# Performance work log

Hardware: AMD Instinct MI355X
Metric: run time of the kernel (lower is better)

The kernel has to match this reference:

```python
import jax, jax.numpy as jnp
import numpy as np

R, C, CH, BA = 2048, 1024, 8, 8
EPS = 1e-10


def setup_inputs() -> dict:
    key = jax.random.key(0)
    k1, k2, k3 = jax.random.split(key, 3)
    # kaiming_uniform_ on [R, CH*BA]: fan_in = CH*BA, bound = sqrt(6/fan_in)
    bound = float(np.sqrt(6.0 / (CH * BA)))
    W = jax.random.uniform(k1, (R, CH * BA), jnp.float32, -bound, bound)
    D = (jax.random.uniform(k2, (R, C)) < 0.1).astype(jnp.float32)
    # Gumbel(0,1) noise, replicating the torch quirk: -log(eps - log(u + eps))
    u = jax.random.uniform(k3, (R, CH * BA), jnp.float32)
    g = -jnp.log(EPS - jnp.log(u + EPS))
    return {"W": W, "D": D, "g": g, "i": 100}


def reference(W, D, g, i):
    # temp = 1000 - 999/3999*i is computed in torch but GumbelSoftmax.forward
    # ignores it and always uses temperature=1, so i has no effect on the math.
    P = jax.nn.softmax(W + g, axis=-1).reshape(R, CH, BA)        # [R,CH,BA]
    x = P[:, None, :, :] * D[:, :, None, None]                    # [R,C,CH,BA]

    nnz_ch_ba = jnp.sum(x, axis=(0, 1))                           # [CH,BA]
    max_nnz_ch = jnp.max(nnz_ch_ba, axis=-1)                      # [CH] (torch dim=2 on 2D -> last axis)

    col_ch = 1.0 - jnp.prod(jnp.prod(1.0 - x, axis=0), axis=2)    # [C,CH]
    num_col_ch = jnp.sum(col_ch, axis=0)                          # [CH]
    num_row_ch = jnp.sum(P, axis=(0, 2))                          # [CH]

    col_density_ch = jnp.sum(
        jnp.sum(x, axis=(0, 3)) / num_row_ch / num_col_ch, axis=0)  # [CH]

    tot_ch = max_nnz_ch + num_col_ch + num_row_ch                 # [CH]

    num_row_sel = jnp.sum(
        (jnp.max(P.reshape(R, -1), axis=1) > 0.99).astype(jnp.float32))
    return (P, tot_ch, max_nnz_ch, num_col_ch, num_row_ch,
            nnz_ch_ba, col_density_ch, num_row_sel)
```

## Files before the change

### kernel.cpp

```cpp
#include <hip/hip_runtime.h>
#include <math.h>

#define R 2048
#define C 1024
#define CH 8
#define K 64

#define OFF_P     0
#define OFF_TOT   (R*K)
#define OFF_MAX   (OFF_TOT + 8)
#define OFF_NCOL  (OFF_MAX + 8)
#define OFF_NROW  (OFF_NCOL + 8)
#define OFF_NNZ   (OFF_NROW + 8)
#define OFF_DEN   (OFF_NNZ + 64)
#define OFF_SEL   (OFF_DEN + 8)

#define WS_LQ   0
#define WS_COL  16384
#define WS_NP   24576
#define WS_NR   40960
#define WS_SEL  43008

__global__ __launch_bounds__(512) void k1(
    const float* __restrict__ W, const float* __restrict__ Dm,
    const float* __restrict__ g, float* __restrict__ P,
    float* __restrict__ ws)
{
    const int tid  = threadIdx.x;
    const int lane = tid & 63;
    const int w    = tid >> 6;
    const int row  = blockIdx.x * 8 + w;

    if (tid < 32) ws[WS_COL + blockIdx.x * 32 + tid] = 0.0f;

    float z = W[row * K + lane] + g[row * K + lane];
    float m = z;
    #pragma unroll
    for (int off = 32; off >= 1; off >>= 1)
        m = fmaxf(m, __shfl_xor(m, off, 64));
    float e = __expf(z - m);
    float s = e;
    #pragma unroll
    for (int off = 32; off >= 1; off >>= 1)
        s += __shfl_xor(s, off, 64);
    float p = e * __builtin_amdgcn_rcpf(s);
    P[row * K + lane] = p;

    const float4* Drow = (const float4*)(Dm + (size_t)row * C);
    float ds = 0.0f;
    #pragma unroll
    for (int j = 0; j < 4; ++j) {
        float4 v = Drow[lane + 64 * j];
        ds += (v.x + v.y) + (v.z + v.w);
    }
    #pragma unroll
    for (int off = 32; off >= 1; off >>= 1)
        ds += __shfl_xor(ds, off, 64);

    float om = 1.0f - p, sc = p;
    #pragma unroll
    for (int off = 1; off <= 4; off <<= 1) {
        om *= __shfl_xor(om, off, 64);
        sc += __shfl_xor(sc, off, 64);
    }
    if ((lane & 7) == 0)
        ws[WS_LQ + row * CH + (lane >> 3)] =
            fmaxf(__builtin_amdgcn_logf(om), -1.0e30f);

    float pm = p;
    #pragma unroll
    for (int off = 32; off >= 1; off >>= 1)
        pm = fmaxf(pm, __shfl_xor(pm, off, 64));

    __shared__ float rn[8][64];
    __shared__ float rp[8][8];
    __shared__ float rsel[8];
    rn[w][lane] = p * ds;
    if ((lane & 7) == 0) rp[w][lane >> 3] = sc;
    if (lane == 0) rsel[w] = (pm > 0.99f) ? 1.0f : 0.0f;
    __syncthreads();

    if (tid < 64) {
        float v = rn[0][tid] + rn[1][tid] + rn[2][tid] + rn[3][tid]
                + rn[4][tid] + rn[5][tid] + rn[6][tid] + rn[7][tid];
        ws[WS_NP + blockIdx.x * 64 + tid] = v;
    }
    if (tid < 8) {
        float v = 0.0f;
        #pragma unroll
        for (int ww = 0; ww < 8; ++ww) v += rp[ww][tid];
        ws[WS_NR + blockIdx.x * 8 + tid] = v;
    }
    if (tid == 0) {
        float v = 0.0f;
        #pragma unroll
        for (int ww = 0; ww < 8; ++ww) v += rsel[ww];
        ws[WS_SEL + blockIdx.x] = v;
    }
}

__global__ __launch_bounds__(256) void k2(
    const float* __restrict__ Dm, float* __restrict__ ws)
{
    const int tid = threadIdx.x;
    const int ct  = blockIdx.x & 3;
    const int rc  = blockIdx.x >> 2;
    const int col = ct * 256 + tid;

    float l0=0,l1=0,l2=0,l3=0,l4=0,l5=0,l6=0,l7=0;
    const int r0 = rc * 32;
    #pragma unroll 4
    for (int i = 0; i < 32; ++i) {
        const int r = r0 + i;
        float d = Dm[(size_t)r * C + col];
        const float* lr = ws + WS_LQ + r * CH;
        l0 += d * lr[0]; l1 += d * lr[1]; l2 += d * lr[2]; l3 += d * lr[3];
        l4 += d * lr[4]; l5 += d * lr[5]; l6 += d * lr[6]; l7 += d * lr[7];
    }
    float* ca = ws + WS_COL;
    atomicAdd(&ca[0 * 1024 + col], l0);
    atomicAdd(&ca[1 * 1024 + col], l1);
    atomicAdd(&ca[2 * 1024 + col], l2);
    atomicAdd(&ca[3 * 1024 + col], l3);
    atomicAdd(&ca[4 * 1024 + col], l4);
    atomicAdd(&ca[5 * 1024 + col], l5);
    atomicAdd(&ca[6 * 1024 + col], l6);
    atomicAdd(&ca[7 * 1024 + col], l7);
}

__global__ __launch_bounds__(1024) void k3(const float* __restrict__ ws,
                                           float* __restrict__ out)
{
    const int tid = threadIdx.x;
    __shared__ float red[1024];
    __shared__ float npr[16][64];
    __shared__ float nrr[8][8];
    __shared__ float selr[64];
    __shared__ float nc8[8];

    {
        const int ch = tid >> 7, c0 = tid & 127;
        float ncl = 0.0f;
        #pragma unroll
        for (int j = 0; j < 8; ++j)
            ncl += 1.0f - __builtin_amdgcn_exp2f(
                              ws[WS_COL + ch * 1024 + j * 128 + c0]);
        red[tid] = ncl;
    }
    {
        const int l = tid & 63, grp = tid >> 6;
        float v = 0.0f;
        #pragma unroll
        for (int b = 0; b < 16; ++b)
            v += ws[WS_NP + (grp * 16 + b) * 64 + l];
        npr[grp][l] = v;
    }
    if (tid < 64) {
        const int ch = tid & 7, grp = tid >> 3;
        float v = 0.0f;
        #pragma unroll
        for (int b = 0; b < 32; ++b)
            v += ws[WS_NR + (grp * 32 + b) * CH + ch];
        nrr[grp][ch] = v;
        float sv = 0.0f;
        #pragma unroll
        for (int j = 0; j < 4; ++j)
            sv += ws[WS_SEL + j * 64 + tid];
        selr[tid] = sv;
    }
    __syncthreads();

    #pragma unroll
    for (int off = 64; off >= 1; off >>= 1) {
        if ((tid & 127) < off) red[tid] += red[tid + off];
        __syncthreads();
    }
    if ((tid & 127) == 0) nc8[tid >> 7] = red[tid];
    __syncthreads();

    if (tid < 64) {
        float nnzv = 0.0f;
        #pragma unroll
        for (int g2 = 0; g2 < 16; ++g2) nnzv += npr[g2][tid];
        out[OFF_NNZ + tid] = nnzv;

        float sum = nnzv, mx = nnzv;
        #pragma unroll
        for (int off = 1; off <= 4; off <<= 1) {
            sum += __shfl_xor(sum, off, 64);
            mx = fmaxf(mx, __shfl_xor(mx, off, 64));
        }
        float sv = selr[tid];
        #pragma unroll
        for (int off = 32; off >= 1; off >>= 1)
            sv += __shfl_xor(sv, off, 64);
        if (tid == 0) out[OFF_SEL] = sv;

        if ((tid & 7) == 0) {
            const int ch = tid >> 3;
            float nr = 0.0f;
            #pragma unroll
            for (int g2 = 0; g2 < 8; ++g2) nr += nrr[g2][ch];
            const float nc = nc8[ch];
            out[OFF_TOT  + ch] = mx + nc + nr;
            out[OFF_MAX  + ch] = mx;
            out[OFF_NCOL + ch] = nc;
            out[OFF_NROW + ch] = nr;
            out[OFF_DEN  + ch] = sum / nr / nc;
        }
    }
}

extern "C" void kernel_launch(void* const* d_in, const int* in_sizes, int n_in,
                              void* d_out, int out_size, void* d_ws, size_t ws_size,
                              hipStream_t stream) {
    const float* W = (const float*)d_in[0];
    const float* D = (const float*)d_in[1];
    const float* g = (const float*)d_in[2];
    float* out = (float*)d_out;
    float* ws  = (float*)d_ws;

    k1<<<256, 512, 0, stream>>>(W, D, g, out, ws);
    k2<<<256, 256, 0, stream>>>(D, ws);
    k3<<<1,  1024, 0, stream>>>(ws, out);
}
```

Baseline: 76.60 us.

## Fuse final reduction into k2 via last-block atomic counter, halve atomics

Removes the third kernel launch by having the last block of k2 (detected through an agent-scope atomic ticket counter reset in k1) perform the final reductions. k2 now uses 512 threads with two row halves combined in shared memory before the global atomicAdds, which halves the number of atomics, and the atomic channel order is staggered per block to spread contention. The final reduction uses wave shuffles instead of a shared-memory tree. This saves a launch and its gap but puts a serial tail on one block and relies on the counter being correctly ordered with the column atomics.

```diff
diff --git a/kernel.cpp b/kernel.cpp
--- a/kernel.cpp
+++ b/kernel.cpp
@@ -20,6 +20,7 @@
 #define WS_NP   24576
 #define WS_NR   40960
 #define WS_SEL  43008
+#define WS_CNT  43264
 
 __global__ __launch_bounds__(512) void k1(
     const float* __restrict__ W, const float* __restrict__ Dm,
@@ -32,6 +33,7 @@
     const int row  = blockIdx.x * 8 + w;
 
     if (tid < 32) ws[WS_COL + blockIdx.x * 32 + tid] = 0.0f;
+    if (blockIdx.x == 0 && tid == 32) ((unsigned*)ws)[WS_CNT] = 0u;
 
     float z = W[row * K + lane] + g[row * K + lane];
     float m = z;
@@ -99,69 +101,90 @@
     }
 }
 
-__global__ __launch_bounds__(256) void k2(
-    const float* __restrict__ Dm, float* __restrict__ ws)
+__global__ __launch_bounds__(512) void k2(
+    const float* __restrict__ Dm, float* __restrict__ ws,
+    float* __restrict__ out)
 {
-    const int tid = threadIdx.x;
-    const int ct  = blockIdx.x & 3;
-    const int rc  = blockIdx.x >> 2;
-    const int col = ct * 256 + tid;
-
-    float l0=0,l1=0,l2=0,l3=0,l4=0,l5=0,l6=0,l7=0;
-    const int r0 = rc * 32;
-    #pragma unroll 4
-    for (int i = 0; i < 32; ++i) {
+    const int tid  = threadIdx.x;
+    const int ct   = blockIdx.x & 3;
+    const int rc   = blockIdx.x >> 2;
+    const int c    = tid & 255;
+    const int col  = ct * 256 + c;
+    const int half = tid >> 8;
+
+    const int r0 = __builtin_amdgcn_readfirstlane(rc * 32 + half * 16);
+
+    float l[8] = {0,0,0,0,0,0,0,0};
+    #pragma unroll
+    for (int i = 0; i < 16; ++i) {
         const int r = r0 + i;
-        float d = Dm[(size_t)r * C + col];
+        const float d = Dm[(size_t)r * C + col];
         const float* lr = ws + WS_LQ + r * CH;
-        l0 += d * lr[0]; l1 += d * lr[1]; l2 += d * lr[2]; l3 += d * lr[3];
-        l4 += d * lr[4]; l5 += d * lr[5]; l6 += d * lr[6]; l7 += d * lr[7];
-    }
-    float* ca = ws + WS_COL;
-    atomicAdd(&ca[0 * 1024 + col], l0);
-    atomicAdd(&ca[1 * 1024 + col], l1);
-    atomicAdd(&ca[2 * 1024 + col], l2);
-    atomicAdd(&ca[3 * 1024 + col], l3);
-    atomicAdd(&ca[4 * 1024 + col], l4);
-    atomicAdd(&ca[5 * 1024 + col], l5);
-    atomicAdd(&ca[6 * 1024 + col], l6);
-    atomicAdd(&ca[7 * 1024 + col], l7);
-}
-
-__global__ __launch_bounds__(1024) void k3(const float* __restrict__ ws,
-                                           float* __restrict__ out)
-{
-    const int tid = threadIdx.x;
-    __shared__ float red[1024];
-    __shared__ float npr[16][64];
+        #pragma unroll
+        for (int j = 0; j < 8; ++j) l[j] += d * lr[j];
+    }
+
+    __shared__ float comb[8][256];
+    if (half) {
+        #pragma unroll
+        for (int j = 0; j < 8; ++j) comb[j][c] = l[j];
+    }
+    __syncthreads();
+    if (!half) {
+        float* ca = ws + WS_COL;
+        const int st = rc & 7;
+        #pragma unroll
+        for (int jj = 0; jj < 8; ++jj) {
+            const int j = (jj + st) & 7;
+            atomicAdd(&ca[j * 1024 + col], l[j] + comb[j][c]);
+        }
+    }
+    __syncthreads();
+
+    __shared__ int amLast;
+    if (tid == 0) {
+        unsigned old = __hip_atomic_fetch_add(
+            (unsigned*)ws + WS_CNT, 1u,
+            __ATOMIC_ACQ_REL, __HIP_MEMORY_SCOPE_AGENT);
+        amLast = (old == 255u);
+    }
+    __syncthreads();
+    if (!amLast) return;
+
+    const int fl = tid & 63;
+    const int fw = tid >> 6;
+
+    __shared__ float nc8[8];
+    __shared__ float npr[8][64];
     __shared__ float nrr[8][8];
     __shared__ float selr[64];
-    __shared__ float nc8[8];
 
     {
-        const int ch = tid >> 7, c0 = tid & 127;
         float ncl = 0.0f;
         #pragma unroll
-        for (int j = 0; j < 8; ++j)
-            ncl += 1.0f - __builtin_amdgcn_exp2f(
-                              ws[WS_COL + ch * 1024 + j * 128 + c0]);
-        red[tid] = ncl;
+        for (int j = 0; j < 16; ++j) {
+            float sv = ws[WS_COL + fw * 1024 + j * 64 + fl];
+            ncl += 1.0f - __builtin_amdgcn_exp2f(sv);
+        }
+        #pragma unroll
+        for (int off = 32; off >= 1; off >>= 1)
+            ncl += __shfl_xor(ncl, off, 64);
+        if (fl == 0) nc8[fw] = ncl;
     }
     {
-        const int l = tid & 63, grp = tid >> 6;
-        float v = 0.0f;
-        #pragma unroll
-        for (int b = 0; b < 16; ++b)
-            v += ws[WS_NP + (grp * 16 + b) * 64 + l];
-        npr[grp][l] = v;
+        float v = 0.0f;
+        #pragma unroll
+        for (int b = 0; b < 32; ++b)
+            v += ws[WS_NP + (fw * 32 + b) * 64 + fl];
+        npr[fw][fl] = v;
     }
     if (tid < 64) {
-        const int ch = tid & 7, grp = tid >> 3;
+        const int ch2 = tid & 7, grp = tid >> 3;
         float v = 0.0f;
         #pragma unroll
         for (int b = 0; b < 32; ++b)
-            v += ws[WS_NR + (grp * 32 + b) * CH + ch];
-        nrr[grp][ch] = v;
+            v += ws[WS_NR + (grp * 32 + b) * CH + ch2];
+        nrr[grp][ch2] = v;
         float sv = 0.0f;
         #pragma unroll
         for (int j = 0; j < 4; ++j)
@@ -170,18 +193,10 @@
     }
     __syncthreads();
 
-    #pragma unroll
-    for (int off = 64; off >= 1; off >>= 1) {
-        if ((tid & 127) < off) red[tid] += red[tid + off];
-        __syncthreads();
-    }
-    if ((tid & 127) == 0) nc8[tid >> 7] = red[tid];
-    __syncthreads();
-
     if (tid < 64) {
         float nnzv = 0.0f;
         #pragma unroll
-        for (int g2 = 0; g2 < 16; ++g2) nnzv += npr[g2][tid];
+        for (int g2 = 0; g2 < 8; ++g2) nnzv += npr[g2][tid];
         out[OFF_NNZ + tid] = nnzv;
 
         float sum = nnzv, mx = nnzv;
@@ -221,6 +236,5 @@
     float* ws  = (float*)d_ws;
 
     k1<<<256, 512, 0, stream>>>(W, D, g, out, ws);
-    k2<<<256, 256, 0, stream>>>(D, ws);
-    k3<<<1,  1024, 0, stream>>>(ws, out);
+    k2<<<256, 512, 0, stream>>>(D, ws, out);
 }
```

New measurement: 78.58 us. 1.03x slower.
